# Kernel optimization log

Measured on AMD Instinct MI355X. Metric: run time of the kernel, lower is better.

The kernel has to match this reference:

```python
import jax, jax.numpy as jnp
import numpy as np

B, F, N_COMP, DEGREE = 8192, 4096, 512, 3
GAMMA = 1.0  # coef0 = 0.0 -> no bias column


def setup_inputs() -> dict:
    key = jax.random.key(0)
    k1, k2, k3 = jax.random.split(key, 3)
    X = jax.random.normal(k1, (B, F), dtype=jnp.float32)
    index_hash = jax.random.randint(k2, (DEGREE, F), 0, N_COMP, dtype=jnp.int32)
    bit_hash = jax.random.randint(k3, (DEGREE, F), 0, 2, dtype=jnp.int32)  # 0/1 -> mapped to +-1
    return {"X": X, "index_hash": index_hash, "bit_hash": bit_hash}


def reference(X, index_hash, bit_hash):
    # CountSketch per degree + TensorSketch product via rFFT.
    sgn = (bit_hash * 2 - 1).astype(X.dtype)          # [D, F] in {-1, +1}
    X_ext = X * (GAMMA ** 0.5)                        # [B, F]

    def count_sketch(idx_d, sgn_d):
        # scatter-add hashed, signed features into N_COMP buckets (per batch row)
        vals = X_ext * sgn_d                          # [B, F]
        return jnp.zeros((X.shape[0], N_COMP), X.dtype).at[:, idx_d].add(vals)

    sketches = jax.vmap(count_sketch)(index_hash, sgn)  # [D, B, N]
    Fr = jnp.fft.rfft(sketches, axis=-1)                # [D, B, N//2+1]
    prod = jnp.prod(Fr, axis=0)                         # [B, N//2+1]
    return jnp.fft.irfft(prod, n=N_COMP, axis=-1)       # [B, N]
```

## Files before the change

### kernel.cpp

```cpp
#include <hip/hip_runtime.h>
#include <math.h>


#define F_DIM 4096
#define NC 512
#define DEG 3
#define THREADS 256
#define PI_F 3.14159265358979323846f

#define OFS_STRIDE 520
#define ENT_BYTE_OFF 4096

__device__ __forceinline__ float2 cmul(float2 a, float2 b) {
    return make_float2(a.x * b.x - a.y * b.y, a.x * b.y + a.y * b.x);
}

__global__ __launch_bounds__(512) void build_csr(
    const int* __restrict__ idxh,
    const int* __restrict__ bith,
    ushort* __restrict__ ofs_g,
    ushort* __restrict__ ent_g)
{
    __shared__ unsigned cnt[NC];
    __shared__ unsigned scn[NC];
    const int d = blockIdx.x;
    const int t = threadIdx.x;

    if (t < NC) cnt[t] = 0;
    __syncthreads();
    for (int f = t; f < F_DIM; f += 512)
        atomicAdd(&cnt[idxh[d * F_DIM + f]], 1u);
    __syncthreads();

    if (t < NC) scn[t] = cnt[t];
    __syncthreads();
    for (int off = 1; off < NC; off <<= 1) {
        unsigned v = 0;
        if (t < NC) { v = scn[t]; if (t >= off) v += scn[t - off]; }
        __syncthreads();
        if (t < NC) scn[t] = v;
        __syncthreads();
    }

    if (t < NC) {
        const unsigned excl = t ? scn[t - 1] : 0u;
        ofs_g[d * OFS_STRIDE + t] = (ushort)excl;
        cnt[t] = excl;
    }
    if (t == 0) ofs_g[d * OFS_STRIDE + NC] = (ushort)F_DIM;
    __syncthreads();

    for (int f = t; f < F_DIM; f += 512) {
        const int b = idxh[d * F_DIM + f];
        const unsigned pos = atomicAdd(&cnt[b], 1u);
        ent_g[d * F_DIM + pos] = (ushort)(f | (bith[d * F_DIM + f] << 15));
    }
}

__global__ __launch_bounds__(THREADS, 2) void ts_kernel(
    const float* __restrict__ X,
    const ushort* __restrict__ ofs_g,
    const ushort* __restrict__ ent_g,
    float* __restrict__ out)
{
    __shared__ float2 sk[4][DEG][NC];
    __shared__ float2 xst[F_DIM];
    float2* tw = xst;

    const int tid  = threadIdx.x;
    const int lane = tid & 63;
    const int wave = tid >> 6;

    int je0[DEG][2], je1[DEG][2];
    #pragma unroll
    for (int d = 0; d < DEG; ++d)
        #pragma unroll
        for (int h = 0; h < 2; ++h) {
            const int b = tid + (h << 8);
            je0[d][h] = ofs_g[d * OFS_STRIDE + b];
            je1[d][h] = ofs_g[d * OFS_STRIDE + b + 1];
        }

    for (int p = 0; p < 4; ++p) {
        const int r0 = blockIdx.x * 8 + p * 2;
        const float* X0 = X + (size_t)r0 * F_DIM;
        const float* X1 = X0 + F_DIM;
        #pragma unroll 4
        for (int i = tid; i < F_DIM; i += THREADS)
            xst[i] = make_float2(X0[i], X1[i]);
        __syncthreads();

        #pragma unroll
        for (int d = 0; d < DEG; ++d)
            #pragma unroll
            for (int h = 0; h < 2; ++h) {
                const int b = tid + (h << 8);
                const ushort* ep = ent_g + d * F_DIM;
                float ax = 0.0f, ay = 0.0f;
                int e = je0[d][h];
                const int eend = je1[d][h];
                for (; e + 4 <= eend; e += 4) {
                    const ushort u0 = ep[e], u1 = ep[e + 1], u2 = ep[e + 2], u3 = ep[e + 3];
                    const float2 v0 = xst[u0 & 4095], v1 = xst[u1 & 4095];
                    const float2 v2 = xst[u2 & 4095], v3 = xst[u3 & 4095];
                    const float s0 = (u0 & 0x8000) ? 1.0f : -1.0f;
                    const float s1 = (u1 & 0x8000) ? 1.0f : -1.0f;
                    const float s2 = (u2 & 0x8000) ? 1.0f : -1.0f;
                    const float s3 = (u3 & 0x8000) ? 1.0f : -1.0f;
                    ax += s0 * v0.x + s1 * v1.x + s2 * v2.x + s3 * v3.x;
                    ay += s0 * v0.y + s1 * v1.y + s2 * v2.y + s3 * v3.y;
                }
                for (; e < eend; ++e) {
                    const ushort u = ep[e];
                    const float2 v = xst[u & 4095];
                    const float s = (u & 0x8000) ? 1.0f : -1.0f;
                    ax += s * v.x; ay += s * v.y;
                }
                sk[p][d][b] = make_float2(ax, ay);
            }
        __syncthreads();
    }

    #pragma unroll
    for (int t = lane; t < NC / 2; t += 64) {
        float sv, cv;
        __sincosf(-2.0f * PI_F * (float)t / (float)NC, &sv, &cv);
        tw[t] = make_float2(cv, sv);
    }

    for (int s = 0; s < 9; ++s) {
        const int h = 256 >> s;
        #pragma unroll
        for (int d = 0; d < DEG; ++d) {
            float2* z = sk[wave][d];
            #pragma unroll
            for (int it = 0; it < 4; ++it) {
                const int u  = lane + (it << 6);
                const int j  = u & (h - 1);
                const int g  = u >> (8 - s);
                const int i1 = (g << (9 - s)) + j;
                const int i2 = i1 + h;
                float2 a = z[i1], b = z[i2];
                float2 t = make_float2(a.x - b.x, a.y - b.y);
                z[i1] = make_float2(a.x + b.x, a.y + b.y);
                z[i2] = cmul(t, tw[j << s]);
            }
        }
    }

    float2 P0[8], P1[8];
    #pragma unroll
    for (int it = 0; it < 8; ++it) {
        const int j  = lane + (it << 6);
        const int k  = (int)(__brev((unsigned)j) >> 23);
        const int kp = (NC - k) & (NC - 1);
        const int jp = (int)(__brev((unsigned)kp) >> 23);
        float2 p0 = make_float2(1.0f, 0.0f);
        float2 p1 = make_float2(1.0f, 0.0f);
        #pragma unroll
        for (int d = 0; d < DEG; ++d) {
            float2 zk = sk[wave][d][j];
            float2 zp = sk[wave][d][jp];
            float2 A  = make_float2(0.5f * (zk.x + zp.x), 0.5f * (zk.y - zp.y));
            float2 Bv = make_float2(0.5f * (zk.y + zp.y), 0.5f * (zp.x - zk.x));
            p0 = cmul(p0, A);
            p1 = cmul(p1, Bv);
        }
        P0[it] = p0;
        P1[it] = p1;
    }
    #pragma unroll
    for (int it = 0; it < 8; ++it) {
        const int j = lane + (it << 6);
        sk[wave][0][j] = make_float2(P0[it].x - P1[it].y, P0[it].y + P1[it].x);
    }

    for (int s = 0; s < 9; ++s) {
        const int h = 1 << s;
        float2* z = sk[wave][0];
        #pragma unroll
        for (int it = 0; it < 4; ++it) {
            const int u  = lane + (it << 6);
            const int j  = u & (h - 1);
            const int g  = u >> s;
            const int i1 = (g << (s + 1)) + j;
            const int i2 = i1 + h;
            float2 a = z[i1];
            float2 w = tw[j << (8 - s)];
            w.y = -w.y;
            float2 b = cmul(z[i2], w);
            z[i1] = make_float2(a.x + b.x, a.y + b.y);
            z[i2] = make_float2(a.x - b.x, a.y - b.y);
        }
    }

    const float scale = 1.0f / (float)NC;
    const int r0 = blockIdx.x * 8 + wave * 2;
    #pragma unroll
    for (int it = 0; it < 8; ++it) {
        const int n = lane + (it << 6);
        const float2 q = sk[wave][0][n];
        out[(size_t)r0 * NC + n]       = q.x * scale;
        out[(size_t)(r0 + 1) * NC + n] = q.y * scale;
    }
}

extern "C" void kernel_launch(void* const* d_in, const int* in_sizes, int n_in,
                              void* d_out, int out_size, void* d_ws, size_t ws_size,
                              hipStream_t stream) {
    const float* X    = (const float*)d_in[0];
    const int*   idxh = (const int*)d_in[1];
    const int*   bith = (const int*)d_in[2];
    float*       outp = (float*)d_out;

    ushort* ofs_g = (ushort*)d_ws;
    ushort* ent_g = (ushort*)((char*)d_ws + ENT_BYTE_OFF);

    build_csr<<<DEG, 512, 0, stream>>>(idxh, bith, ofs_g, ent_g);

    const int n_rows = in_sizes[0] / F_DIM;
    const int blocks = n_rows / 8;
    ts_kernel<<<blocks, THREADS, 0, stream>>>(X, ofs_g, ent_g, outp);
}
```

Before: 267.6 us.

## Move per-wave FFTs into registers with shuffles, shrink LDS for higher occupancy

The forward and inverse 512-point FFTs now run in registers: each lane holds 8 elements, does the first stages in-register and the rest through cross-lane xor shuffles, with per-lane twiddles precomputed by sincos instead of an LDS table. The per-pass sketch buffer shrinks to a single shared exchange array, and each wave copies its pass into registers. This cuts LDS use enough to allow 3 blocks per CU instead of 2, and X rows are now loaded with float4. In exchange it adds register pressure from the 24 held complex values plus twiddles, and an extra barrier per pass.

New measurement: 263.2 us. Within noise of the previous version (-1.6%).

```diff
diff --git a/kernel.cpp b/kernel.cpp
--- a/kernel.cpp
+++ b/kernel.cpp
@@ -13,6 +13,38 @@
 
 __device__ __forceinline__ float2 cmul(float2 a, float2 b) {
     return make_float2(a.x * b.x - a.y * b.y, a.x * b.y + a.y * b.x);
+}
+__device__ __forceinline__ float2 cmulc(float2 a, float2 b) {
+    return make_float2(a.x * b.x + a.y * b.y, a.y * b.x - a.x * b.y);
+}
+__device__ __forceinline__ float2 shflx(float2 v, int m) {
+    return make_float2(__shfl_xor(v.x, m), __shfl_xor(v.y, m));
+}
+
+__device__ __forceinline__ void fwd_lane_stage(float2 (&s)[8], int lane, int m, float2 w) {
+    const bool up = (lane & m) != 0;
+    const float sg = up ? -1.0f : 1.0f;
+    const float2 weff = up ? w : make_float2(1.0f, 0.0f);
+    #pragma unroll
+    for (int r = 0; r < 8; ++r) {
+        const float2 zz = s[r];
+        const float2 pp = shflx(zz, m);
+        const float2 dd = make_float2(fmaf(sg, zz.x, pp.x), fmaf(sg, zz.y, pp.y));
+        s[r] = cmul(dd, weff);
+    }
+}
+__device__ __forceinline__ void inv_lane_stage(float2 (&s)[8], int lane, int m, float2 w) {
+    const bool up = (lane & m) != 0;
+    const float sg = up ? -1.0f : 1.0f;
+    #pragma unroll
+    for (int r = 0; r < 8; ++r) {
+        const float2 zz = s[r];
+        const float2 pp = shflx(zz, m);
+        const float2 a  = up ? pp : zz;
+        const float2 bs = up ? zz : pp;
+        const float2 t  = cmulc(bs, w);
+        s[r] = make_float2(fmaf(sg, t.x, a.x), fmaf(sg, t.y, a.y));
+    }
 }
 
 __global__ __launch_bounds__(512) void build_csr(
@@ -57,15 +89,15 @@
     }
 }
 
-__global__ __launch_bounds__(THREADS, 2) void ts_kernel(
+__global__ __launch_bounds__(THREADS, 3) void ts_kernel(
     const float* __restrict__ X,
     const ushort* __restrict__ ofs_g,
     const ushort* __restrict__ ent_g,
     float* __restrict__ out)
 {
-    __shared__ float2 sk[4][DEG][NC];
-    __shared__ float2 xst[F_DIM];
-    float2* tw = xst;
+    __shared__ float4 xst4[F_DIM / 2];
+    __shared__ float2 exch[DEG][NC];
+    float2* xst = (float2*)xst4;
 
     const int tid  = threadIdx.x;
     const int lane = tid & 63;
@@ -81,13 +113,42 @@
             je1[d][h] = ofs_g[d * OFS_STRIDE + b + 1];
         }
 
+    const float wang = -2.0f * PI_F / 512.0f;
+    float2 tw0[4], tw1[2], tw2, tw3, tw4, tw5, tw6, tw7;
+    #pragma unroll
+    for (int c = 0; c < 4; ++c) {
+        float sv, cv; __sincosf(wang * (float)(c * 64 + lane), &sv, &cv);
+        tw0[c] = make_float2(cv, sv);
+    }
+    #pragma unroll
+    for (int c = 0; c < 2; ++c) {
+        float sv, cv; __sincosf(wang * (float)(2 * (c * 64 + lane)), &sv, &cv);
+        tw1[c] = make_float2(cv, sv);
+    }
+    { float sv, cv; __sincosf(wang * (float)(4 * lane),          &sv, &cv); tw2 = make_float2(cv, sv); }
+    { float sv, cv; __sincosf(wang * (float)(8 * (lane & 31)),   &sv, &cv); tw3 = make_float2(cv, sv); }
+    { float sv, cv; __sincosf(wang * (float)(16 * (lane & 15)),  &sv, &cv); tw4 = make_float2(cv, sv); }
+    { float sv, cv; __sincosf(wang * (float)(32 * (lane & 7)),   &sv, &cv); tw5 = make_float2(cv, sv); }
+    { float sv, cv; __sincosf(wang * (float)(64 * (lane & 3)),   &sv, &cv); tw6 = make_float2(cv, sv); }
+    { float sv, cv; __sincosf(wang * (float)(128 * (lane & 1)),  &sv, &cv); tw7 = make_float2(cv, sv); }
+
+    int jp0 = 0;
+    if (lane >= 1) { const int msb = 31 - __builtin_clz((unsigned)lane); jp0 = lane ^ ((1 << msb) - 1); }
+
+    float2 z[DEG][8];
+
     for (int p = 0; p < 4; ++p) {
-        const int r0 = blockIdx.x * 8 + p * 2;
-        const float* X0 = X + (size_t)r0 * F_DIM;
-        const float* X1 = X0 + F_DIM;
-        #pragma unroll 4
-        for (int i = tid; i < F_DIM; i += THREADS)
-            xst[i] = make_float2(X0[i], X1[i]);
+        const int pr0 = blockIdx.x * 8 + p * 2;
+        const float4* X0q = (const float4*)(X + (size_t)pr0 * F_DIM);
+        const float4* X1q = (const float4*)(X + (size_t)(pr0 + 1) * F_DIM);
+        #pragma unroll
+        for (int k = 0; k < 4; ++k) {
+            const int i4 = tid + k * THREADS;
+            const float4 a = X0q[i4];
+            const float4 b = X1q[i4];
+            xst4[2 * i4]     = make_float4(a.x, b.x, a.y, b.y);
+            xst4[2 * i4 + 1] = make_float4(a.z, b.z, a.w, b.w);
+        }
         __syncthreads();
 
         #pragma unroll
@@ -116,92 +177,124 @@
                     const float s = (u & 0x8000) ? 1.0f : -1.0f;
                     ax += s * v.x; ay += s * v.y;
                 }
-                sk[p][d][b] = make_float2(ax, ay);
+                exch[d][b] = make_float2(ax, ay);
             }
         __syncthreads();
-    }
-
-    #pragma unroll
-    for (int t = lane; t < NC / 2; t += 64) {
-        float sv, cv;
-        __sincosf(-2.0f * PI_F * (float)t / (float)NC, &sv, &cv);
-        tw[t] = make_float2(cv, sv);
-    }
-
-    for (int s = 0; s < 9; ++s) {
-        const int h = 256 >> s;
-        #pragma unroll
-        for (int d = 0; d < DEG; ++d) {
-            float2* z = sk[wave][d];
+
+        if (wave == p) {
             #pragma unroll
-            for (int it = 0; it < 4; ++it) {
-                const int u  = lane + (it << 6);
-                const int j  = u & (h - 1);
-                const int g  = u >> (8 - s);
-                const int i1 = (g << (9 - s)) + j;
-                const int i2 = i1 + h;
-                float2 a = z[i1], b = z[i2];
-                float2 t = make_float2(a.x - b.x, a.y - b.y);
-                z[i1] = make_float2(a.x + b.x, a.y + b.y);
-                z[i2] = cmul(t, tw[j << s]);
+            for (int d = 0; d < DEG; ++d)
+                #pragma unroll
+                for (int it = 0; it < 8; ++it)
+                    z[d][it] = exch[d][it * 64 + lane];
+        }
+        __syncthreads();
+    }
+
+    float2 P0[8], P1[8];
+    #pragma unroll
+    for (int it = 0; it < 8; ++it) { P0[it] = make_float2(1.0f, 0.0f); P1[it] = make_float2(1.0f, 0.0f); }
+
+    #pragma unroll
+    for (int d = 0; d < DEG; ++d) {
+        float2 s[8];
+        #pragma unroll
+        for (int it = 0; it < 8; ++it) s[it] = z[d][it];
+
+        #pragma unroll
+        for (int c = 0; c < 4; ++c) {
+            const float2 a = s[c], b = s[c + 4];
+            s[c]     = make_float2(a.x + b.x, a.y + b.y);
+            s[c + 4] = cmul(make_float2(a.x - b.x, a.y - b.y), tw0[c]);
+        }
+        #pragma unroll
+        for (int g = 0; g < 2; ++g)
+            #pragma unroll
+            for (int c = 0; c < 2; ++c) {
+                const int i1 = g * 4 + c, i2 = i1 + 2;
+                const float2 a = s[i1], b = s[i2];
+                s[i1] = make_float2(a.x + b.x, a.y + b.y);
+                s[i2] = cmul(make_float2(a.x - b.x, a.y - b.y), tw1[c]);
             }
-        }
-    }
-
-    float2 P0[8], P1[8];
-    #pragma unroll
-    for (int it = 0; it < 8; ++it) {
-        const int j  = lane + (it << 6);
-        const int k  = (int)(__brev((unsigned)j) >> 23);
-        const int kp = (NC - k) & (NC - 1);
-        const int jp = (int)(__brev((unsigned)kp) >> 23);
-        float2 p0 = make_float2(1.0f, 0.0f);
-        float2 p1 = make_float2(1.0f, 0.0f);
-        #pragma unroll
-        for (int d = 0; d < DEG; ++d) {
-            float2 zk = sk[wave][d][j];
-            float2 zp = sk[wave][d][jp];
-            float2 A  = make_float2(0.5f * (zk.x + zp.x), 0.5f * (zk.y - zp.y));
-            float2 Bv = make_float2(0.5f * (zk.y + zp.y), 0.5f * (zp.x - zk.x));
-            p0 = cmul(p0, A);
-            p1 = cmul(p1, Bv);
-        }
-        P0[it] = p0;
-        P1[it] = p1;
-    }
-    #pragma unroll
-    for (int it = 0; it < 8; ++it) {
-        const int j = lane + (it << 6);
-        sk[wave][0][j] = make_float2(P0[it].x - P1[it].y, P0[it].y + P1[it].x);
-    }
-
-    for (int s = 0; s < 9; ++s) {
-        const int h = 1 << s;
-        float2* z = sk[wave][0];
-        #pragma unroll
-        for (int it = 0; it < 4; ++it) {
-            const int u  = lane + (it << 6);
-            const int j  = u & (h - 1);
-            const int g  = u >> s;
-            const int i1 = (g << (s + 1)) + j;
-            const int i2 = i1 + h;
-            float2 a = z[i1];
-            float2 w = tw[j << (8 - s)];
-            w.y = -w.y;
-            float2 b = cmul(z[i2], w);
-            z[i1] = make_float2(a.x + b.x, a.y + b.y);
-            z[i2] = make_float2(a.x - b.x, a.y - b.y);
-        }
+        #pragma unroll
+        for (int g = 0; g < 4; ++g) {
+            const int i1 = 2 * g, i2 = i1 + 1;
+            const float2 a = s[i1], b = s[i2];
+            s[i1] = make_float2(a.x + b.x, a.y + b.y);
+            s[i2] = cmul(make_float2(a.x - b.x, a.y - b.y), tw2);
+        }
+        fwd_lane_stage(s, lane, 32, tw3);
+        fwd_lane_stage(s, lane, 16, tw4);
+        fwd_lane_stage(s, lane, 8,  tw5);
+        fwd_lane_stage(s, lane, 4,  tw6);
+        fwd_lane_stage(s, lane, 2,  tw7);
+        fwd_lane_stage(s, lane, 1,  make_float2(1.0f, 0.0f));
+
+        float2 zp[8];
+        zp[0] = make_float2(__shfl(s[0].x, jp0), __shfl(s[0].y, jp0));
+        zp[1] = shflx(s[1], 63);
+        zp[2] = shflx(s[3], 63);
+        zp[3] = shflx(s[2], 63);
+        zp[4] = shflx(s[7], 63);
+        zp[5] = shflx(s[6], 63);
+        zp[6] = shflx(s[5], 63);
+        zp[7] = shflx(s[4], 63);
+        #pragma unroll
+        for (int it = 0; it < 8; ++it) {
+            const float2 zk = s[it], zq = zp[it];
+            const float2 A = make_float2(0.5f * (zk.x + zq.x), 0.5f * (zk.y - zq.y));
+            const float2 B = make_float2(0.5f * (zk.y + zq.y), 0.5f * (zq.x - zk.x));
+            P0[it] = cmul(P0[it], A);
+            P1[it] = cmul(P1[it], B);
+        }
+    }
+
+    float2 q[8];
+    #pragma unroll
+    for (int it = 0; it < 8; ++it)
+        q[it] = make_float2(P0[it].x - P1[it].y, P0[it].y + P1[it].x);
+
+    inv_lane_stage(q, lane, 1,  make_float2(1.0f, 0.0f));
+    inv_lane_stage(q, lane, 2,  tw7);
+    inv_lane_stage(q, lane, 4,  tw6);
+    inv_lane_stage(q, lane, 8,  tw5);
+    inv_lane_stage(q, lane, 16, tw4);
+    inv_lane_stage(q, lane, 32, tw3);
+    #pragma unroll
+    for (int g = 0; g < 4; ++g) {
+        const int i1 = 2 * g, i2 = i1 + 1;
+        const float2 a = q[i1];
+        const float2 t = cmulc(q[i2], tw2);
+        q[i1] = make_float2(a.x + t.x, a.y + t.y);
+        q[i2] = make_float2(a.x - t.x, a.y - t.y);
+    }
+    #pragma unroll
+    for (int g = 0; g < 2; ++g)
+        #pragma unroll
+        for (int c = 0; c < 2; ++c) {
+            const int i1 = g * 4 + c, i2 = i1 + 2;
+            const float2 a = q[i1];
+            const float2 t = cmulc(q[i2], tw1[c]);
+            q[i1] = make_float2(a.x + t.x, a.y + t.y);
+            q[i2] = make_float2(a.x - t.x, a.y - t.y);
+        }
+    #pragma unroll
+    for (int c = 0; c < 4; ++c) {
+        const float2 a = q[c];
+        const float2 t = cmulc(q[c + 4], tw0[c]);
+        q[c]     = make_float2(a.x + t.x, a.y + t.y);
+        q[c + 4] = make_float2(a.x - t.x, a.y - t.y);
     }
 
     const float scale = 1.0f / (float)NC;
     const int r0 = blockIdx.x * 8 + wave * 2;
+    float* o0 = out + (size_t)r0 * NC;
+    float* o1 = o0 + NC;
     #pragma unroll
     for (int it = 0; it < 8; ++it) {
-        const int n = lane + (it << 6);
-        const float2 q = sk[wave][0][n];
-        out[(size_t)r0 * NC + n]       = q.x * scale;
-        out[(size_t)(r0 + 1) * NC + n] = q.y * scale;
+        const int n = it * 64 + lane;
+        o0[n] = q[it].x * scale;
+        o1[n] = q[it].y * scale;
     }
 }
 
```
